# Kernel tuning notes

Hardware: AMD Instinct MI355X
Metric: run time of the kernel (lower is better)

## Reference

```python
import jax, jax.numpy as jnp
import numpy as np

V, D, NH, NL, HID = 128000, 512, 8, 2, 1408
HD = D // NH
HALF = HD // 2
B, T, NLAB, LBL = 4, 508, 5, 4
EPS = 1e-5


def setup_inputs() -> dict:
    key = jax.random.key(0)
    ks = jax.random.split(key, 16)
    g = lambda k, sh: (jax.random.normal(k, sh, jnp.float32) * 0.02)
    return {
        "input_ids": jax.random.randint(ks[0], (B, T), 0, V),
        "label_ids": jax.random.randint(ks[1], (NLAB, LBL), 0, V),
        "emb": g(ks[2], (V, D)),
        "wq": g(ks[3], (NL, D, D)),
        "wk": g(ks[4], (NL, D, D)),
        "wv": g(ks[5], (NL, D, D)),
        "wo": g(ks[6], (NL, D, D)),
        "w1": g(ks[7], (NL, D, HID)),
        "w2": g(ks[8], (NL, HID, D)),
        "w3": g(ks[9], (NL, D, HID)),
        "attn_norm_w": jnp.ones((NL, D), jnp.float32),
        "ffn_norm_w": jnp.ones((NL, D), jnp.float32),
        "final_norm_w": jnp.ones((D,), jnp.float32),
        "lm_head": g(ks[10], (D, V)),
    }


def _rmsnorm(x, w):
    return x * jax.lax.rsqrt(jnp.mean(x * x, axis=-1, keepdims=True) + EPS) * w


def _score(input_ids, label_ids, emb, wq, wk, wv, wo, w1, w2, w3,
           attn_norm_w, ffn_norm_w, final_norm_w, lm_head):
    Bc, Tc = input_ids.shape
    nl, Lc = label_ids.shape
    S = Tc + Lc
    # pad_id is None in the original (tokenizer attr missing) -> all lengths == T.
    # Causal attention => one forward over [prefix || label] equals the per-token re-forwards.
    ctx = jnp.concatenate([
        jnp.broadcast_to(input_ids[None], (nl, Bc, Tc)),
        jnp.broadcast_to(label_ids[:, None, :], (nl, Bc, Lc)),
    ], axis=-1).reshape(nl * Bc, S)
    N = nl * Bc

    h = emb[ctx]  # [N, S, D]

    # RoPE tables
    pos = jnp.arange(S, dtype=jnp.float32)
    freqs = 1.0 / (10000.0 ** (jnp.arange(HALF, dtype=jnp.float32) / HALF))
    ang = pos[:, None] * freqs[None, :]  # [S, HALF]
    cos = jnp.cos(ang)[None, :, None, :]
    sin = jnp.sin(ang)[None, :, None, :]

    def rope(x):  # x: [N, S, NH, HD]
        x1, x2 = x[..., :HALF], x[..., HALF:]
        return jnp.concatenate([x1 * cos - x2 * sin, x1 * sin + x2 * cos], axis=-1)

    causal = jnp.tril(jnp.ones((S, S), dtype=bool))
    scale = 1.0 / jnp.sqrt(jnp.float32(HD))

    for l in range(NL):
        xn = _rmsnorm(h, attn_norm_w[l])
        q = rope((xn @ wq[l]).reshape(N, S, NH, HD))
        k = rope((xn @ wk[l]).reshape(N, S, NH, HD))
        v = (xn @ wv[l]).reshape(N, S, NH, HD)
        scores = jnp.einsum('nqhd,nkhd->nhqk', q, k) * scale
        scores = jnp.where(causal, scores, jnp.float32(-1e9))
        p = jax.nn.softmax(scores, axis=-1)
        o = jnp.einsum('nhqk,nkhd->nqhd', p, v).reshape(N, S, D)
        h = h + o @ wo[l]
        xn = _rmsnorm(h, ffn_norm_w[l])
        h = h + (jax.nn.silu(xn @ w1[l]) * (xn @ w3[l])) @ w2[l]

    h = _rmsnorm(h, final_norm_w)
    # Only positions T-1 .. T+L-2 predict label tokens; project only those.
    hs = h[:, Tc - 1:Tc - 1 + Lc, :]                    # [N, L, D]
    lp = jax.nn.log_softmax(hs @ lm_head, axis=-1)      # [N, L, V]
    lp = lp.reshape(nl, Bc, Lc, V)
    idx = jnp.broadcast_to(label_ids[:, None, :, None], (nl, Bc, Lc, 1))
    tok_lp = jnp.take_along_axis(lp, idx, axis=-1)[..., 0]  # [nl, B, L]
    return tok_lp.sum(axis=-1).T.astype(jnp.float32)        # [B, num_labels]


def reference(input_ids, label_ids, emb, wq, wk, wv, wo, w1, w2, w3,
              attn_norm_w, ffn_norm_w, final_norm_w, lm_head):
    return _score(input_ids, label_ids, emb, wq, wk, wv, wo, w1, w2, w3,
                  attn_norm_w, ffn_norm_w, final_norm_w, lm_head)
```

## Files before the change

kernel.cpp:

```cpp
#include <hip/hip_runtime.h>
#include <math.h>

typedef unsigned short u16;
typedef unsigned int u32;

namespace {
constexpr int kV = 128000, kD = 512, kNH = 8, kNL = 2, kHID = 1408;
constexpr int kHD = 64, kB = 4, kT = 508, kNLAB = 5, kLBL = 4;
constexpr int kS = 512;
constexpr int kNSeq = kNLAB * kB;
constexpr int kNS = kNSeq * kS;
constexpr int kQK = 1024;
constexpr float kEps = 1e-5f;
constexpr int kNChunk = 2000;
constexpr int kPad = 56;
constexpr int kStr = 72;
constexpr int kPL = 3211264;
constexpr int oWQ = 0, oWK = 262144, oWV = 524288, oWO = 786432;
constexpr int oW1 = 1048576, oW3 = 1769472, oW2 = 2490368;
}

typedef __attribute__((ext_vector_type(8))) short bf16x8;
typedef __attribute__((ext_vector_type(4))) float f32x4;

__device__ inline u32 pk2(float lo, float hi) {
  u32 ul = __builtin_bit_cast(u32, lo);
  u32 uh = __builtin_bit_cast(u32, hi);
  ul += 0x7fffu + ((ul >> 16) & 1u);
  uh += 0x7fffu + ((uh >> 16) & 1u);
  return (ul >> 16) | (uh & 0xffff0000u);
}
__device__ inline u16 bf1(float x) {
  u32 u = __builtin_bit_cast(u32, x);
  u += 0x7fffu + ((u >> 16) & 1u);
  return (u16)(u >> 16);
}
__device__ inline float bf2f(u16 u) {
  return __builtin_bit_cast(float, ((u32)u) << 16);
}
__device__ inline void gload16(const void* g, void* l) {
  __builtin_amdgcn_global_load_lds(
      (const __attribute__((address_space(1))) void*)g,
      (__attribute__((address_space(3))) void*)l, 16, 0, 0);
}
__device__ inline size_t tix(int Kt, int row, int k) {
  return ((size_t)(row >> 7) * Kt + (k >> 6)) * 8192 +
         ((((k >> 4) & 3) * 2 + ((k >> 3) & 1)) * 128 + (row & 127)) * 8 + (k & 7);
}

__global__ __launch_bounds__(256) void k_wtrans_all(const float* __restrict__ wq,
                                                    const float* __restrict__ wk,
                                                    const float* __restrict__ wv,
                                                    const float* __restrict__ wo,
                                                    const float* __restrict__ w1,
                                                    const float* __restrict__ w3,
                                                    const float* __restrict__ w2,
                                                    u16* __restrict__ wT) {
  int bid = blockIdx.x;
  int l = bid / 3136, r = bid % 3136;
  const float* src; u16* dst; int K, N, gxw, t; float scale = 1.f;
  if (r < 1024) {
    int w = r >> 8; t = r & 255; K = 512; N = 512; gxw = 16;
    src = (w == 0 ? wq : w == 1 ? wk : w == 2 ? wv : wo) + (size_t)l * 262144;
    dst = wT + (size_t)l * kPL + w * 262144;
    if (w == 0) scale = 0.125f;
  } else if (r < 2432) {
    int rr = r - 1024; int w = rr / 704; t = rr - w * 704; K = 512; N = 1408; gxw = 44;
    src = (w ? w3 : w1) + (size_t)l * 720896;
    dst = wT + (size_t)l * kPL + (w ? oW3 : oW1);
  } else {
    t = r - 2432; K = 1408; N = 512; gxw = 16;
    src = w2 + (size_t)l * 720896;
    dst = wT + (size_t)l * kPL + oW2;
  }
  int bn = (t % gxw) * 32, bk = (t / gxw) * 32;
  __shared__ float tb[32][33];
  int tid = threadIdx.x;
  int rr2 = tid >> 3, c4 = (tid & 7) * 4;
  float4 v = *(const float4*)(src + (size_t)(bk + rr2) * N + bn + c4);
  tb[rr2][c4 + 0] = v.x * scale; tb[rr2][c4 + 1] = v.y * scale;
  tb[rr2][c4 + 2] = v.z * scale; tb[rr2][c4 + 3] = v.w * scale;
  __syncthreads();
  uint2 o;
  o.x = pk2(tb[c4 + 0][rr2], tb[c4 + 1][rr2]);
  o.y = pk2(tb[c4 + 2][rr2], tb[c4 + 3][rr2]);
  *(uint2*)&dst[tix(K >> 6, bn + rr2, bk + c4)] = o;
}

__global__ void k_embed(const int* __restrict__ input_ids, const int* __restrict__ label_ids,
                        const float* __restrict__ emb, float* __restrict__ h) {
  int row = blockIdx.x;
  int n = row / kS, s = row - n * kS;
  int lab = n / kB, b = n - lab * kB;
  int tok = (s < kT) ? input_ids[b * kT + s] : label_ids[lab * kLBL + (s - kT)];
  const float4* src = (const float4*)(emb + (size_t)tok * kD);
  float4* dst = (float4*)(h + (size_t)row * kD);
  for (int i = threadIdx.x; i < kD / 4; i += blockDim.x) dst[i] = src[i];
}

__global__ __launch_bounds__(256) void k_rmsnorm(const float* __restrict__ x,
                                                 const float* __restrict__ w,
                                                 u16* __restrict__ y) {
  int row = blockIdx.x;
  int tid = threadIdx.x;
  const float* xr = x + (size_t)row * kD;
  int i = tid * 2;
  float v0 = xr[i], v1 = xr[i + 1];
  float ss = v0 * v0 + v1 * v1;
  #pragma unroll
  for (int o = 1; o < 64; o <<= 1) ss += __shfl_xor(ss, o);
  __shared__ float wsum[4];
  int lane = tid & 63, wid = tid >> 6;
  if (lane == 0) wsum[wid] = ss;
  __syncthreads();
  float tot = wsum[0] + wsum[1] + wsum[2] + wsum[3];
  float inv = rsqrtf(tot / (float)kD + kEps);
  *(u32*)&y[tix(8, row, i)] = pk2(v0 * inv * w[i], v1 * inv * w[i + 1]);
}

__global__ __launch_bounds__(256) void k_gemm_qkv(const u16* __restrict__ A,
                                                  const u16* __restrict__ Bt,
                                                  u16* __restrict__ qk,
                                                  u16* __restrict__ vT) {
  __shared__ u16 As[8192];
  __shared__ u16 Bs[8192];
  int wg = (blockIdx.x & 7) * 120 + (blockIdx.x >> 3);
  int by = wg / 12, bx = wg - by * 12;
  int row0 = by * 128, col0 = bx * 128;
  int tid = threadIdx.x;
  int wave = tid >> 6, lane = tid & 63;
  int wm = wave >> 1, wn = wave & 1;
  int l15 = lane & 15, l16 = lane >> 4;
  f32x4 acc[4][4];
  #pragma unroll
  for (int i = 0; i < 4; i++)
    #pragma unroll
    for (int j = 0; j < 4; j++) acc[i][j] = (f32x4){0.f, 0.f, 0.f, 0.f};

  for (int kt = 0; kt < 8; kt++) {
    const u16* Ab = A  + ((size_t)(row0 >> 7) * 8 + kt) * 8192;
    const u16* Bb = Bt + ((size_t)(col0 >> 7) * 8 + kt) * 8192;
    #pragma unroll
    for (int i = 0; i < 4; i++) {
      int off = ((wave * 2 + (i >> 1)) * 128 + (i & 1) * 64) * 8;
      gload16(Ab + off + (size_t)lane * 8, (char*)As + off * 2);
      gload16(Bb + off + (size_t)lane * 8, (char*)Bs + off * 2);
    }
    __syncthreads();
    #pragma unroll
    for (int h = 0; h < 2; h++) {
      bf16x8 af[4], bfr[4];
      #pragma unroll
      for (int mf = 0; mf < 4; mf++)
        af[mf] = *(const bf16x8*)&As[((h * 4 + l16) * 128 + wm * 64 + mf * 16 + l15) * 8];
      #pragma unroll
      for (int nf = 0; nf < 4; nf++)
        bfr[nf] = *(const bf16x8*)&Bs[((h * 4 + l16) * 128 + wn * 64 + nf * 16 + l15) * 8];
      #pragma unroll
      for (int mf = 0; mf < 4; mf++)
        #pragma unroll
        for (int nf = 0; nf < 4; nf++)
          acc[mf][nf] = __builtin_amdgcn_mfma_f32_16x16x32_bf16(af[mf], bfr[nf], acc[mf][nf], 0, 0, 0);
    }
    __syncthreads();
  }

  if (bx < 8) {
    #pragma unroll
    for (int nf = 0; nf < 2; nf++) {
      int d = nf * 16 + l15;
      float fr = __expf(-0.2878231366242558f * (float)d);
      #pragma unroll
      for (int mf = 0; mf < 4; mf++)
        #pragma unroll
        for (int r = 0; r < 4; r++) {
          int row = row0 + wm * 64 + mf * 16 + l16 * 4 + r;
          int s = row & (kS - 1);
          float sn, cs;
          __sincosf((float)s * fr, &sn, &cs);
          float x1 = acc[mf][nf][r], x2 = acc[mf][nf + 2][r];
          size_t base = (size_t)row * kQK + col0 + wn * 64 + nf * 16 + l15;
          qk[base]      = bf1(x1 * cs - x2 * sn);
          qk[base + 32] = bf1(x1 * sn + x2 * cs);
        }
    }
  } else {
    int n = row0 >> 9;
    #pragma unroll
    for (int mf = 0; mf < 4; mf++) {
      int s0 = (row0 & (kS - 1)) + wm * 64 + mf * 16 + l16 * 4;
      #pragma unroll
      for (int nf = 0; nf < 4; nf++) {
        int v = (bx - 8) * 128 + wn * 64 + nf * 16 + l15;
        int hh = v >> 6, d = v & 63;
        uint2 ow;
        ow.x = pk2(acc[mf][nf][0], acc[mf][nf][1]);
        ow.y = pk2(acc[mf][nf][2], acc[mf][nf][3]);
        *(uint2*)&vT[(size_t)((n * kNH + hh) * kHD + d) * kS + s0] = ow;
      }
    }
  }
}

__global__ __launch_bounds__(256) void k_gemm_n64(const u16* __restrict__ A,
                                                  const u16* __restrict__ Bt,
                                                  float* __restrict__ C,
                                                  int Kt, int N) {
  __shared__ u16 As[8192];
  __shared__ u16 Bs[4096];
  int nwg = gridDim.x;
  int wg = (blockIdx.x & 7) * (nwg >> 3) + (blockIdx.x >> 3);
  int by = wg >> 3, bx = wg & 7;
  int row0 = by * 128, col0 = bx * 64;
  int p = col0 >> 7, half = (col0 >> 6) & 1;
  int tid = threadIdx.x;
  int wave = tid >> 6, lane = tid & 63;
  int l15 = lane & 15, l16 = lane >> 4;
  f32x4 acc[2][4];
  #pragma unroll
  for (int i = 0; i < 2; i++)
    #pragma unroll
    for (int j = 0; j < 4; j++) acc[i][j] = (f32x4){0.f, 0.f, 0.f, 0.f};

  for (int kt = 0; kt < Kt; kt++) {
    const u16* Ab = A  + ((size_t)(row0 >> 7) * Kt + kt) * 8192;
    const u16* Bb = Bt + ((size_t)p * Kt + kt) * 8192;
    #pragma unroll
    for (int i = 0; i < 4; i++) {
      int off = ((wave * 2 + (i >> 1)) * 128 + (i & 1) * 64) * 8;
      gload16(Ab + off + (size_t)lane * 8, (char*)As + off * 2);
    }
    #pragma unroll
    for (int sl = 0; sl < 2; sl++) {
      int ch = wave * 2 + sl;
      gload16(Bb + (ch * 128 + half * 64) * 8 + (size_t)lane * 8,
              (char*)Bs + (ch * 64) * 16);
    }
    __syncthreads();
    #pragma unroll
    for (int h = 0; h < 2; h++) {
      bf16x8 af[2], bfr[4];
      #pragma unroll
      for (int mf = 0; mf < 2; mf++)
        af[mf] = *(const bf16x8*)&As[((h * 4 + l16) * 128 + wave * 32 + mf * 16 + l15) * 8];
      #pragma unroll
      for (int nf = 0; nf < 4; nf++)
        bfr[nf] = *(const bf16x8*)&Bs[((h * 4 + l16) * 64 + nf * 16 + l15) * 8];
      #pragma unroll
      for (int mf = 0; mf < 2; mf++)
        #pragma unroll
        for (int nf = 0; nf < 4; nf++)
          acc[mf][nf] = __builtin_amdgcn_mfma_f32_16x16x32_bf16(af[mf], bfr[nf], acc[mf][nf], 0, 0, 0);
    }
    __syncthreads();
  }
  #pragma unroll
  for (int mf = 0; mf < 2; mf++)
    #pragma unroll
    for (int nf = 0; nf < 4; nf++)
      #pragma unroll
      for (int r = 0; r < 4; r++) {
        int row = row0 + wave * 32 + mf * 16 + l16 * 4 + r;
        int col = col0 + nf * 16 + l15;
        C[(size_t)row * N + col] += acc[mf][nf][r];
      }
}

__global__ __launch_bounds__(256) void k_ffn13_bf16(const u16* __restrict__ A,
                                                    const u16* __restrict__ W1t,
                                                    const u16* __restrict__ W3t,
                                                    u16* __restrict__ act) {
  __shared__ u16 As[8192];
  __shared__ u16 B1[8192];
  __shared__ u16 B2[8192];
  int wg = (blockIdx.x & 7) * 110 + (blockIdx.x >> 3);
  int by = wg / 11, bx = wg - by * 11;
  int row0 = by * 128, col0 = bx * 128;
  int tid = threadIdx.x;
  int wave = tid >> 6, lane = tid & 63;
  int wm = wave >> 1, wn = wave & 1;
  int l15 = lane & 15, l16 = lane >> 4;
  f32x4 acc1[4][4], acc2[4][4];
  #pragma unroll
  for (int i = 0; i < 4; i++)
    #pragma unroll
    for (int j = 0; j < 4; j++) {
      acc1[i][j] = (f32x4){0.f, 0.f, 0.f, 0.f};
      acc2[i][j] = (f32x4){0.f, 0.f, 0.f, 0.f};
    }

  for (int kt = 0; kt < 8; kt++) {
    const u16* Ab  = A   + ((size_t)(row0 >> 7) * 8 + kt) * 8192;
    const u16* B1b = W1t + ((size_t)(col0 >> 7) * 8 + kt) * 8192;
    const u16* B3b = W3t + ((size_t)(col0 >> 7) * 8 + kt) * 8192;
    #pragma unroll
    for (int i = 0; i < 4; i++) {
      int off = ((wave * 2 + (i >> 1)) * 128 + (i & 1) * 64) * 8;
      gload16(Ab  + off + (size_t)lane * 8, (char*)As + off * 2);
      gload16(B1b + off + (size_t)lane * 8, (char*)B1 + off * 2);
      gload16(B3b + off + (size_t)lane * 8, (char*)B2 + off * 2);
    }
    __syncthreads();
    #pragma unroll
    for (int h = 0; h < 2; h++) {
      bf16x8 af[4], b1f[4], b2f[4];
      #pragma unroll
      for (int mf = 0; mf < 4; mf++)
        af[mf] = *(const bf16x8*)&As[((h * 4 + l16) * 128 + wm * 64 + mf * 16 + l15) * 8];
      #pragma unroll
      for (int nf = 0; nf < 4; nf++) {
        b1f[nf] = *(const bf16x8*)&B1[((h * 4 + l16) * 128 + wn * 64 + nf * 16 + l15) * 8];
        b2f[nf] = *(const bf16x8*)&B2[((h * 4 + l16) * 128 + wn * 64 + nf * 16 + l15) * 8];
      }
      #pragma unroll
      for (int mf = 0; mf < 4; mf++)
        #pragma unroll
        for (int nf = 0; nf < 4; nf++) {
          acc1[mf][nf] = __builtin_amdgcn_mfma_f32_16x16x32_bf16(af[mf], b1f[nf], acc1[mf][nf], 0, 0, 0);
          acc2[mf][nf] = __builtin_amdgcn_mfma_f32_16x16x32_bf16(af[mf], b2f[nf], acc2[mf][nf], 0, 0, 0);
        }
    }
    __syncthreads();
  }
  #pragma unroll
  for (int mf = 0; mf < 4; mf++)
    #pragma unroll
    for (int nf = 0; nf < 4; nf++)
      #pragma unroll
      for (int r = 0; r < 4; r++) {
        int row = row0 + wm * 64 + mf * 16 + l16 * 4 + r;
        int col = col0 + wn * 64 + nf * 16 + l15;
        float aa = acc1[mf][nf][r];
        float sg = 1.f / (1.f + __expf(-aa));
        act[tix(22, row, col)] = bf1(aa * sg * acc2[mf][nf][r]);
      }
}

__global__ __launch_bounds__(256) void k_attn_mfma(const u16* __restrict__ qk,
                                                   const u16* __restrict__ vT,
                                                   u16* __restrict__ o) {
  int qt = blockIdx.x;
  int nh = blockIdx.y;
  int hh = nh & (kNH - 1), n = nh >> 3;
  int tid = threadIdx.x;
  int wq = tid >> 6, lane = tid & 63;
  int l15 = lane & 15, l16 = lane >> 4;
  __shared__ u16 Ks[64 * kStr];
  __shared__ u16 Vt[64 * kStr];
  __shared__ u16 Ps[4][16 * kStr];
  int q0 = qt * 64;
  int qrow = q0 + wq * 16 + l15;

  bf16x8 qf[2];
  {
    const u16* qg = qk + (size_t)(n * kS + qrow) * kQK + hh * kHD;
    qf[0] = *(const bf16x8*)(qg + l16 * 8);
    qf[1] = *(const bf16x8*)(qg + 32 + l16 * 8);
  }

  f32x4 oacc[4];
  #pragma unroll
  for (int i = 0; i < 4; i++) oacc[i] = (f32x4){0.f, 0.f, 0.f, 0.f};
  float m_run = -1e30f, l_run = 0.f;

  int skv = tid & 63, sd0 = (tid >> 6) * 16;
  const u16* vTh = vT + (size_t)((n * kNH + hh) * kHD) * kS;

  for (int jt = 0; jt <= qt; jt++) {
    int j0 = jt * 64;
    __syncthreads();
    {
      size_t gb = (size_t)(n * kS + j0 + skv) * kQK + 512 + hh * kHD + sd0;
      const u16* kg = qk + gb;
      *(uint4*)&Ks[skv * kStr + sd0]     = *(const uint4*)kg;
      *(uint4*)&Ks[skv * kStr + sd0 + 8] = *(const uint4*)(kg + 8);
      const u16* vg = vTh + (size_t)skv * kS + j0 + sd0;
      *(uint4*)&Vt[skv * kStr + sd0]     = *(const uint4*)vg;
      *(uint4*)&Vt[skv * kStr + sd0 + 8] = *(const uint4*)(vg + 8);
    }
    __syncthreads();

    f32x4 st[4];
    #pragma unroll
    for (int kt = 0; kt < 4; kt++) {
      bf16x8 ka0 = *(const bf16x8*)&Ks[(kt * 16 + l15) * kStr + l16 * 8];
      bf16x8 ka1 = *(const bf16x8*)&Ks[(kt * 16 + l15) * kStr + 32 + l16 * 8];
      f32x4 c = (f32x4){0.f, 0.f, 0.f, 0.f};
      c = __builtin_amdgcn_mfma_f32_16x16x32_bf16(ka0, qf[0], c, 0, 0, 0);
      c = __builtin_amdgcn_mfma_f32_16x16x32_bf16(ka1, qf[1], c, 0, 0, 0);
      st[kt] = c;
    }

    float mx = m_run;
    #pragma unroll
    for (int kt = 0; kt < 4; kt++)
      #pragma unroll
      for (int r = 0; r < 4; r++) {
        int kvg = j0 + kt * 16 + l16 * 4 + r;
        if (kvg > qrow) st[kt][r] = -1e30f;
        mx = fmaxf(mx, st[kt][r]);
      }
    mx = fmaxf(mx, __shfl_xor(mx, 16));
    mx = fmaxf(mx, __shfl_xor(mx, 32));
    float sc = __expf(m_run - mx);
    float p[4][4];
    float rs = 0.f;
    #pragma unroll
    for (int kt = 0; kt < 4; kt++)
      #pragma unroll
      for (int r = 0; r < 4; r++) { p[kt][r] = __expf(st[kt][r] - mx); rs += p[kt][r]; }
    rs += __shfl_xor(rs, 16);
    rs += __shfl_xor(rs, 32);
    l_run = l_run * sc + rs;
    m_run = mx;
    #pragma unroll
    for (int dt = 0; dt < 4; dt++)
      #pragma unroll
      for (int r = 0; r < 4; r++) oacc[dt][r] *= sc;

    #pragma unroll
    for (int kt = 0; kt < 4; kt++) {
      uint2 w2;
      w2.x = pk2(p[kt][0], p[kt][1]);
      w2.y = pk2(p[kt][2], p[kt][3]);
      *(uint2*)&Ps[wq][l15 * kStr + kt * 16 + l16 * 4] = w2;
    }
    asm volatile("s_waitcnt lgkmcnt(0)" ::: "memory");
    __builtin_amdgcn_sched_barrier(0);

    bf16x8 pf0 = *(const bf16x8*)&Ps[wq][l15 * kStr + l16 * 8];
    bf16x8 pf1 = *(const bf16x8*)&Ps[wq][l15 * kStr + 32 + l16 * 8];
    #pragma unroll
    for (int dt = 0; dt < 4; dt++) {
      bf16x8 va0 = *(const bf16x8*)&Vt[(dt * 16 + l15) * kStr + l16 * 8];
      bf16x8 va1 = *(const bf16x8*)&Vt[(dt * 16 + l15) * kStr + 32 + l16 * 8];
      oacc[dt] = __builtin_amdgcn_mfma_f32_16x16x32_bf16(va0, pf0, oacc[dt], 0, 0, 0);
      oacc[dt] = __builtin_amdgcn_mfma_f32_16x16x32_bf16(va1, pf1, oacc[dt], 0, 0, 0);
    }
  }

  float inv = 1.f / l_run;
  int rowIdx = n * kS + qrow;
  #pragma unroll
  for (int dt = 0; dt < 4; dt++) {
    uint2 ow;
    ow.x = pk2(oacc[dt][0] * inv, oacc[dt][1] * inv);
    ow.y = pk2(oacc[dt][2] * inv, oacc[dt][3] * inv);
    size_t base = ((size_t)(rowIdx >> 7) * 8 + hh) * 8192 +
                  (size_t)(((dt * 2 + ((l16 >> 1) & 1)) * 128 + (rowIdx & 127)) * 8 + (l16 & 1) * 4);
    *(uint2*)&o[base] = ow;
  }
}

__global__ __launch_bounds__(256) void k_rms_gather(const float* __restrict__ x,
                                                    const float* __restrict__ w,
                                                    u16* __restrict__ hs) {
  int r = blockIdx.x;
  int n = r >> 2, li = r & 3;
  int row = n * kS + (kT - 1 + li);
  int tid = threadIdx.x;
  const float* xr = x + (size_t)row * kD;
  int i = tid * 2;
  float v0 = xr[i], v1 = xr[i + 1];
  float ss = v0 * v0 + v1 * v1;
  #pragma unroll
  for (int o = 1; o < 64; o <<= 1) ss += __shfl_xor(ss, o);
  __shared__ float wsum[4];
  int lane = tid & 63, wid = tid >> 6;
  if (lane == 0) wsum[wid] = ss;
  __syncthreads();
  float tot = wsum[0] + wsum[1] + wsum[2] + wsum[3];
  float inv = rsqrtf(tot / (float)kD + kEps);
  *(u32*)&hs[(size_t)r * kD + i] = pk2(v0 * inv * w[i], v1 * inv * w[i + 1]);
}

__global__ __launch_bounds__(256) void k_logits_mfma(const u16* __restrict__ hs,
                                                     const float* __restrict__ lm,
                                                     float* __restrict__ part) {
  __shared__ u16 As[80 * kPad];
  __shared__ u16 Bs[4 * 256 * 8];
  int tid = threadIdx.x;
  int wave = tid >> 6, lane = tid & 63;
  int l15 = lane & 15, l16 = lane >> 4;
  int col0 = blockIdx.x * 256;
  f32x4 acc[5][4];
  #pragma unroll
  for (int i = 0; i < 5; i++)
    #pragma unroll
    for (int j = 0; j < 4; j++) acc[i][j] = (f32x4){0.f, 0.f, 0.f, 0.f};

  int arow = tid >> 1, ahalf = tid & 1;
  int bkp = tid >> 4, bf4 = tid & 15;
  int slot = bkp >> 2, ksub = (2 * bkp) & 7;

  for (int k0 = 0; k0 < kD; k0 += 32) {
    if (tid < 160) {
      const u16* ag = hs + (size_t)arow * kD + k0 + ahalf * 16;
      *(uint4*)&As[arow * kPad + ahalf * 16]     = *(const uint4*)ag;
      *(uint4*)&As[arow * kPad + ahalf * 16 + 8] = *(const uint4*)(ag + 8);
    }
    #pragma unroll
    for (int t = 0; t < 4; t++) {
      int colq = bf4 + 16 * t;
      const float* bg = lm + (size_t)(k0 + 2 * bkp) * kV + col0 + colq * 4;
      float4 lo = *(const float4*)bg;
      float4 hi = *(const float4*)(bg + kV);
      *(u32*)&Bs[(slot * 256 + colq * 4 + 0) * 8 + ksub] = pk2(lo.x, hi.x);
      *(u32*)&Bs[(slot * 256 + colq * 4 + 1) * 8 + ksub] = pk2(lo.y, hi.y);
      *(u32*)&Bs[(slot * 256 + colq * 4 + 2) * 8 + ksub] = pk2(lo.z, hi.z);
      *(u32*)&Bs[(slot * 256 + colq * 4 + 3) * 8 + ksub] = pk2(lo.w, hi.w);
    }
    __syncthreads();
    bf16x8 af[5], bfr[4];
    #pragma unroll
    for (int mf = 0; mf < 5; mf++)
      af[mf] = *(const bf16x8*)&As[(mf * 16 + l15) * kPad + l16 * 8];
    #pragma unroll
    for (int nf = 0; nf < 4; nf++)
      bfr[nf] = *(const bf16x8*)&Bs[(l16 * 256 + wave * 64 + nf * 16 + l15) * 8];
    #pragma unroll
    for (int mf = 0; mf < 5; mf++)
      #pragma unroll
      for (int nf = 0; nf < 4; nf++)
        acc[mf][nf] = __builtin_amdgcn_mfma_f32_16x16x32_bf16(af[mf], bfr[nf], acc[mf][nf], 0, 0, 0);
    __syncthreads();
  }

  int chunk = blockIdx.x * 4 + wave;
  #pragma unroll
  for (int mf = 0; mf < 5; mf++)
    #pragma unroll
    for (int r = 0; r < 4; r++) {
      float mx = fmaxf(fmaxf(acc[mf][0][r], acc[mf][1][r]),
                       fmaxf(acc[mf][2][r], acc[mf][3][r]));
      #pragma unroll
      for (int off = 1; off < 16; off <<= 1) mx = fmaxf(mx, __shfl_xor(mx, off));
      float se = expf(acc[mf][0][r] - mx) + expf(acc[mf][1][r] - mx) +
                 expf(acc[mf][2][r] - mx) + expf(acc[mf][3][r] - mx);
      #pragma unroll
      for (int off = 1; off < 16; off <<= 1) se += __shfl_xor(se, off);
      if (l15 == 0) {
        int row = mf * 16 + l16 * 4 + r;
        size_t pi = ((size_t)row * kNChunk + chunk) * 2;
        part[pi] = mx; part[pi + 1] = se;
      }
    }
}

__global__ __launch_bounds__(64) void k_final(const float* __restrict__ part,
                                              const u16* __restrict__ hs,
                                              const float* __restrict__ lm,
                                              const int* __restrict__ label_ids,
                                              float* __restrict__ out) {
  int n = blockIdx.x;
  int lab = n / kB, b = n - lab * kB;
  int lane = threadIdx.x;
  float res = 0.f;
  for (int li = 0; li < kLBL; li++) {
    int r = n * kLBL + li;
    int tok = label_ids[lab * kLBL + li];
    float dv = 0.f;
    for (int d2 = lane; d2 < kD; d2 += 64)
      dv += bf2f(hs[(size_t)r * kD + d2]) * lm[(size_t)d2 * kV + tok];
    #pragma unroll
    for (int o2 = 1; o2 < 64; o2 <<= 1) dv += __shfl_xor(dv, o2);
    const float* pr = part + (size_t)r * kNChunk * 2;
    float mx = -1e30f;
    for (int c = lane; c < kNChunk; c += 64) mx = fmaxf(mx, pr[c * 2]);
    #pragma unroll
    for (int o2 = 1; o2 < 64; o2 <<= 1) mx = fmaxf(mx, __shfl_xor(mx, o2));
    float sum = 0.f;
    for (int c = lane; c < kNChunk; c += 64) sum += pr[c * 2 + 1] * expf(pr[c * 2] - mx);
    #pragma unroll
    for (int o2 = 1; o2 < 64; o2 <<= 1) sum += __shfl_xor(sum, o2);
    res += dv - (mx + logf(sum));
  }
  if (lane == 0) out[b * kNLAB + lab] = res;
}

extern "C" void kernel_launch(void* const* d_in, const int* in_sizes, int n_in,
                              void* d_out, int out_size, void* d_ws, size_t ws_size,
                              hipStream_t stream) {
  const int*   input_ids    = (const int*)d_in[0];
  const int*   label_ids    = (const int*)d_in[1];
  const float* emb          = (const float*)d_in[2];
  const float* wq           = (const float*)d_in[3];
  const float* wk           = (const float*)d_in[4];
  const float* wv           = (const float*)d_in[5];
  const float* wo           = (const float*)d_in[6];
  const float* w1           = (const float*)d_in[7];
  const float* w2           = (const float*)d_in[8];
  const float* w3           = (const float*)d_in[9];
  const float* attn_norm_w  = (const float*)d_in[10];
  const float* ffn_norm_w   = (const float*)d_in[11];
  const float* final_norm_w = (const float*)d_in[12];
  const float* lm_head      = (const float*)d_in[13];
  float* out = (float*)d_out;

  char* ws = (char*)d_ws;
  float* h    = (float*)(ws);
  u16*   xn   = (u16*)(ws + 20971520);
  u16*   qk   = (u16*)(ws + 31457280);
  u16*   vT   = (u16*)(ws + 52428800);
  u16*   big  = (u16*)(ws + 62914560);
  u16*   hsb  = (u16*)(ws + 91750400);
  float* part = (float*)(ws + 91832320);
  u16*   wT   = (u16*)(ws + 93112640);

  k_wtrans_all<<<2 * 3136, 256, 0, stream>>>(wq, wk, wv, wo, w1, w3, w2, wT);
  k_embed<<<kNS, 128, 0, stream>>>(input_ids, label_ids, emb, h);

  for (int l = 0; l < kNL; l++) {
    u16* base = wT + (size_t)l * kPL;
    k_rmsnorm<<<kNS, 256, 0, stream>>>(h, attn_norm_w + (size_t)l * kD, xn);
    k_gemm_qkv<<<960, 256, 0, stream>>>(xn, base + oWQ, qk, vT);
    dim3 gattn(kS / 64, kNSeq * kNH);
    k_attn_mfma<<<gattn, 256, 0, stream>>>(qk, vT, big);
    k_gemm_n64<<<640, 256, 0, stream>>>(big, base + oWO, h, 8, kD);
    k_rmsnorm<<<kNS, 256, 0, stream>>>(h, ffn_norm_w + (size_t)l * kD, xn);
    k_ffn13_bf16<<<880, 256, 0, stream>>>(xn, base + oW1, base + oW3, big);
    k_gemm_n64<<<640, 256, 0, stream>>>(big, base + oW2, h, 22, kD);
  }

  k_rms_gather<<<kNSeq * kLBL, 256, 0, stream>>>(h, final_norm_w, hsb);
  k_logits_mfma<<<kV / 256, 256, 0, stream>>>(hsb, lm_head, part);
  k_final<<<kNSeq, 64, 0, stream>>>(part, hsb, lm_head, label_ids, out);
}
```

Baseline: 529.2 us.

## Fuse embedding with first RMSNorm, widen attention q-tile, narrow logits tiles

Three unrelated changes. The embedding gather now also computes the first attention RMSNorm, which removes one full pass over h. The attention kernel now gives each wave 32 query rows, so one K/V tile load in shared memory serves twice as many rows, at the cost of fewer blocks and more registers. The logits kernel uses 128-column tiles instead of 256, doubling the block count (and the partial chunk buffer) to improve occupancy, with the workspace offset moved to fit.

```diff
diff --git a/kernel.cpp b/kernel.cpp
--- a/kernel.cpp
+++ b/kernel.cpp
@@ -12,7 +12,7 @@
 constexpr int kNS = kNSeq * kS;
 constexpr int kQK = 1024;
 constexpr float kEps = 1e-5f;
-constexpr int kNChunk = 2000;
+constexpr int kNChunk = 4000;
 constexpr int kPad = 56;
 constexpr int kStr = 72;
 constexpr int kPL = 3211264;
@@ -87,15 +87,31 @@
   *(uint2*)&dst[tix(K >> 6, bn + rr2, bk + c4)] = o;
 }
 
-__global__ void k_embed(const int* __restrict__ input_ids, const int* __restrict__ label_ids,
-                        const float* __restrict__ emb, float* __restrict__ h) {
+__global__ __launch_bounds__(256) void k_embed_rms(const int* __restrict__ input_ids,
+                                                   const int* __restrict__ label_ids,
+                                                   const float* __restrict__ emb,
+                                                   const float* __restrict__ w,
+                                                   float* __restrict__ h,
+                                                   u16* __restrict__ xn) {
   int row = blockIdx.x;
   int n = row / kS, s = row - n * kS;
   int lab = n / kB, b = n - lab * kB;
   int tok = (s < kT) ? input_ids[b * kT + s] : label_ids[lab * kLBL + (s - kT)];
-  const float4* src = (const float4*)(emb + (size_t)tok * kD);
-  float4* dst = (float4*)(h + (size_t)row * kD);
-  for (int i = threadIdx.x; i < kD / 4; i += blockDim.x) dst[i] = src[i];
+  int tid = threadIdx.x;
+  const float* src = emb + (size_t)tok * kD;
+  int i = tid * 2;
+  float v0 = src[i], v1 = src[i + 1];
+  float ss = v0 * v0 + v1 * v1;
+  #pragma unroll
+  for (int o = 1; o < 64; o <<= 1) ss += __shfl_xor(ss, o);
+  __shared__ float wsum[4];
+  int lane = tid & 63, wid = tid >> 6;
+  if (lane == 0) wsum[wid] = ss;
+  __syncthreads();
+  float tot = wsum[0] + wsum[1] + wsum[2] + wsum[3];
+  float inv = rsqrtf(tot / (float)kD + kEps);
+  *(float2*)&h[(size_t)row * kD + i] = make_float2(v0, v1);
+  *(u32*)&xn[tix(8, row, i)] = pk2(v0 * inv * w[i], v1 * inv * w[i + 1]);
 }
 
 __global__ __launch_bounds__(256) void k_rmsnorm(const float* __restrict__ x,
@@ -339,7 +355,7 @@
 __global__ __launch_bounds__(256) void k_attn_mfma(const u16* __restrict__ qk,
                                                    const u16* __restrict__ vT,
                                                    u16* __restrict__ o) {
-  int qt = blockIdx.x;
+  int qb = blockIdx.x;
   int nh = blockIdx.y;
   int hh = nh & (kNH - 1), n = nh >> 3;
   int tid = threadIdx.x;
@@ -347,26 +363,29 @@
   int l15 = lane & 15, l16 = lane >> 4;
   __shared__ u16 Ks[64 * kStr];
   __shared__ u16 Vt[64 * kStr];
-  __shared__ u16 Ps[4][16 * kStr];
-  int q0 = qt * 64;
-  int qrow = q0 + wq * 16 + l15;
-
-  bf16x8 qf[2];
-  {
-    const u16* qg = qk + (size_t)(n * kS + qrow) * kQK + hh * kHD;
-    qf[0] = *(const bf16x8*)(qg + l16 * 8);
-    qf[1] = *(const bf16x8*)(qg + 32 + l16 * 8);
-  }
-
-  f32x4 oacc[4];
-  #pragma unroll
-  for (int i = 0; i < 4; i++) oacc[i] = (f32x4){0.f, 0.f, 0.f, 0.f};
-  float m_run = -1e30f, l_run = 0.f;
+  __shared__ u16 Ps[4][32 * kStr];
+  int qbase = qb * 128 + wq * 32;
+
+  bf16x8 qf[2][2];
+  #pragma unroll
+  for (int g = 0; g < 2; g++) {
+    const u16* qg = qk + (size_t)(n * kS + qbase + g * 16 + l15) * kQK + hh * kHD;
+    qf[g][0] = *(const bf16x8*)(qg + l16 * 8);
+    qf[g][1] = *(const bf16x8*)(qg + 32 + l16 * 8);
+  }
+
+  f32x4 oacc[2][4];
+  #pragma unroll
+  for (int g = 0; g < 2; g++)
+    #pragma unroll
+    for (int i = 0; i < 4; i++) oacc[g][i] = (f32x4){0.f, 0.f, 0.f, 0.f};
+  float m_run[2] = {-1e30f, -1e30f}, l_run[2] = {0.f, 0.f};
 
   int skv = tid & 63, sd0 = (tid >> 6) * 16;
   const u16* vTh = vT + (size_t)((n * kNH + hh) * kHD) * kS;
-
-  for (int jt = 0; jt <= qt; jt++) {
+  int ntile = 2 * qb + 2;
+
+  for (int jt = 0; jt < ntile; jt++) {
     int j0 = jt * 64;
     __syncthreads();
     {
@@ -380,75 +399,88 @@
     }
     __syncthreads();
 
-    f32x4 st[4];
-    #pragma unroll
-    for (int kt = 0; kt < 4; kt++) {
-      bf16x8 ka0 = *(const bf16x8*)&Ks[(kt * 16 + l15) * kStr + l16 * 8];
-      bf16x8 ka1 = *(const bf16x8*)&Ks[(kt * 16 + l15) * kStr + 32 + l16 * 8];
-      f32x4 c = (f32x4){0.f, 0.f, 0.f, 0.f};
-      c = __builtin_amdgcn_mfma_f32_16x16x32_bf16(ka0, qf[0], c, 0, 0, 0);
-      c = __builtin_amdgcn_mfma_f32_16x16x32_bf16(ka1, qf[1], c, 0, 0, 0);
-      st[kt] = c;
-    }
-
-    float mx = m_run;
-    #pragma unroll
-    for (int kt = 0; kt < 4; kt++)
-      #pragma unroll
-      for (int r = 0; r < 4; r++) {
-        int kvg = j0 + kt * 16 + l16 * 4 + r;
-        if (kvg > qrow) st[kt][r] = -1e30f;
-        mx = fmaxf(mx, st[kt][r]);
-      }
-    mx = fmaxf(mx, __shfl_xor(mx, 16));
-    mx = fmaxf(mx, __shfl_xor(mx, 32));
-    float sc = __expf(m_run - mx);
-    float p[4][4];
-    float rs = 0.f;
-    #pragma unroll
-    for (int kt = 0; kt < 4; kt++)
-      #pragma unroll
-      for (int r = 0; r < 4; r++) { p[kt][r] = __expf(st[kt][r] - mx); rs += p[kt][r]; }
-    rs += __shfl_xor(rs, 16);
-    rs += __shfl_xor(rs, 32);
-    l_run = l_run * sc + rs;
-    m_run = mx;
-    #pragma unroll
-    for (int dt = 0; dt < 4; dt++)
-      #pragma unroll
-      for (int r = 0; r < 4; r++) oacc[dt][r] *= sc;
-
-    #pragma unroll
-    for (int kt = 0; kt < 4; kt++) {
-      uint2 w2;
-      w2.x = pk2(p[kt][0], p[kt][1]);
-      w2.y = pk2(p[kt][2], p[kt][3]);
-      *(uint2*)&Ps[wq][l15 * kStr + kt * 16 + l16 * 4] = w2;
+    #pragma unroll
+    for (int g = 0; g < 2; g++) {
+      int qrow = qbase + g * 16 + l15;
+      f32x4 st[4];
+      #pragma unroll
+      for (int kt = 0; kt < 4; kt++) {
+        bf16x8 ka0 = *(const bf16x8*)&Ks[(kt * 16 + l15) * kStr + l16 * 8];
+        bf16x8 ka1 = *(const bf16x8*)&Ks[(kt * 16 + l15) * kStr + 32 + l16 * 8];
+        f32x4 c = (f32x4){0.f, 0.f, 0.f, 0.f};
+        c = __builtin_amdgcn_mfma_f32_16x16x32_bf16(ka0, qf[g][0], c, 0, 0, 0);
+        c = __builtin_amdgcn_mfma_f32_16x16x32_bf16(ka1, qf[g][1], c, 0, 0, 0);
+        st[kt] = c;
+      }
+      float mx = m_run[g];
+      #pragma unroll
+      for (int kt = 0; kt < 4; kt++)
+        #pragma unroll
+        for (int r = 0; r < 4; r++) {
+          int kvg = j0 + kt * 16 + l16 * 4 + r;
+          if (kvg > qrow) st[kt][r] = -1e30f;
+          mx = fmaxf(mx, st[kt][r]);
+        }
+      mx = fmaxf(mx, __shfl_xor(mx, 16));
+      mx = fmaxf(mx, __shfl_xor(mx, 32));
+      float sc = __expf(m_run[g] - mx);
+      float p[4][4];
+      float rs = 0.f;
+      #pragma unroll
+      for (int kt = 0; kt < 4; kt++)
+        #pragma unroll
+        for (int r = 0; r < 4; r++) { p[kt][r] = __expf(st[kt][r] - mx); rs += p[kt][r]; }
+      rs += __shfl_xor(rs, 16);
+      rs += __shfl_xor(rs, 32);
+      l_run[g] = l_run[g] * sc + rs;
+      m_run[g] = mx;
+      #pragma unroll
+      for (int dt = 0; dt < 4; dt++)
+        #pragma unroll
+        for (int r = 0; r < 4; r++) oacc[g][dt][r] *= sc;
+
+      #pragma unroll
+      for (int kt = 0; kt < 4; kt++) {
+        uint2 w2;
+        w2.x = pk2(p[kt][0], p[kt][1]);
+        w2.y = pk2(p[kt][2], p[kt][3]);
+        *(uint2*)&Ps[wq][(g * 16 + l15) * kStr + kt * 16 + l16 * 4] = w2;
+      }
     }
     asm volatile("s_waitcnt lgkmcnt(0)" ::: "memory");
     __builtin_amdgcn_sched_barrier(0);
 
-    bf16x8 pf0 = *(const bf16x8*)&Ps[wq][l15 * kStr + l16 * 8];
-    bf16x8 pf1 = *(const bf16x8*)&Ps[wq][l15 * kStr + 32 + l16 * 8];
+    bf16x8 pf[2][2];
+    #pragma unroll
+    for (int g = 0; g < 2; g++) {
+      pf[g][0] = *(const bf16x8*)&Ps[wq][(g * 16 + l15) * kStr + l16 * 8];
+      pf[g][1] = *(const bf16x8*)&Ps[wq][(g * 16 + l15) * kStr + 32 + l16 * 8];
+    }
     #pragma unroll
     for (int dt = 0; dt < 4; dt++) {
       bf16x8 va0 = *(const bf16x8*)&Vt[(dt * 16 + l15) * kStr + l16 * 8];
       bf16x8 va1 = *(const bf16x8*)&Vt[(dt * 16 + l15) * kStr + 32 + l16 * 8];
-      oacc[dt] = __builtin_amdgcn_mfma_f32_16x16x32_bf16(va0, pf0, oacc[dt], 0, 0, 0);
-      oacc[dt] = __builtin_amdgcn_mfma_f32_16x16x32_bf16(va1, pf1, oacc[dt], 0, 0, 0);
-    }
-  }
-
-  float inv = 1.f / l_run;
-  int rowIdx = n * kS + qrow;
-  #pragma unroll
-  for (int dt = 0; dt < 4; dt++) {
-    uint2 ow;
-    ow.x = pk2(oacc[dt][0] * inv, oacc[dt][1] * inv);
-    ow.y = pk2(oacc[dt][2] * inv, oacc[dt][3] * inv);
-    size_t base = ((size_t)(rowIdx >> 7) * 8 + hh) * 8192 +
-                  (size_t)(((dt * 2 + ((l16 >> 1) & 1)) * 128 + (rowIdx & 127)) * 8 + (l16 & 1) * 4);
-    *(uint2*)&o[base] = ow;
+      #pragma unroll
+      for (int g = 0; g < 2; g++) {
+        oacc[g][dt] = __builtin_amdgcn_mfma_f32_16x16x32_bf16(va0, pf[g][0], oacc[g][dt], 0, 0, 0);
+        oacc[g][dt] = __builtin_amdgcn_mfma_f32_16x16x32_bf16(va1, pf[g][1], oacc[g][dt], 0, 0, 0);
+      }
+    }
+  }
+
+  #pragma unroll
+  for (int g = 0; g < 2; g++) {
+    float inv = 1.f / l_run[g];
+    int rowIdx = n * kS + qbase + g * 16 + l15;
+    #pragma unroll
+    for (int dt = 0; dt < 4; dt++) {
+      uint2 ow;
+      ow.x = pk2(oacc[g][dt][0] * inv, oacc[g][dt][1] * inv);
+      ow.y = pk2(oacc[g][dt][2] * inv, oacc[g][dt][3] * inv);
+      size_t base = ((size_t)(rowIdx >> 7) * 8 + hh) * 8192 +
+                    (size_t)(((dt * 2 + ((l16 >> 1) & 1)) * 128 + (rowIdx & 127)) * 8 + (l16 & 1) * 4);
+      *(uint2*)&o[base] = ow;
+    }
   }
 }
 
@@ -478,16 +510,16 @@
                                                      const float* __restrict__ lm,
                                                      float* __restrict__ part) {
   __shared__ u16 As[80 * kPad];
-  __shared__ u16 Bs[4 * 256 * 8];
+  __shared__ u16 Bs[4 * 128 * 8];
   int tid = threadIdx.x;
   int wave = tid >> 6, lane = tid & 63;
   int l15 = lane & 15, l16 = lane >> 4;
-  int col0 = blockIdx.x * 256;
-  f32x4 acc[5][4];
+  int col0 = blockIdx.x * 128;
+  f32x4 acc[5][2];
   #pragma unroll
   for (int i = 0; i < 5; i++)
     #pragma unroll
-    for (int j = 0; j < 4; j++) acc[i][j] = (f32x4){0.f, 0.f, 0.f, 0.f};
+    for (int j = 0; j < 2; j++) acc[i][j] = (f32x4){0.f, 0.f, 0.f, 0.f};
 
   int arow = tid >> 1, ahalf = tid & 1;
   int bkp = tid >> 4, bf4 = tid & 15;
@@ -500,28 +532,28 @@
       *(uint4*)&As[arow * kPad + ahalf * 16 + 8] = *(const uint4*)(ag + 8);
     }
     #pragma unroll
-    for (int t = 0; t < 4; t++) {
+    for (int t = 0; t < 2; t++) {
       int colq = bf4 + 16 * t;
       const float* bg = lm + (size_t)(k0 + 2 * bkp) * kV + col0 + colq * 4;
       float4 lo = *(const float4*)bg;
       float4 hi = *(const float4*)(bg + kV);
-      *(u32*)&Bs[(slot * 256 + colq * 4 + 0) * 8 + ksub] = pk2(lo.x, hi.x);
-      *(u32*)&Bs[(slot * 256 + colq * 4 + 1) * 8 + ksub] = pk2(lo.y, hi.y);
-      *(u32*)&Bs[(slot * 256 + colq * 4 + 2) * 8 + ksub] = pk2(lo.z, hi.z);
-      *(u32*)&Bs[(slot * 256 + colq * 4 + 3) * 8 + ksub] = pk2(lo.w, hi.w);
-    }
-    __syncthreads();
-    bf16x8 af[5], bfr[4];
+      *(u32*)&Bs[(slot * 128 + colq * 4 + 0) * 8 + ksub] = pk2(lo.x, hi.x);
+      *(u32*)&Bs[(slot * 128 + colq * 4 + 1) * 8 + ksub] = pk2(lo.y, hi.y);
+      *(u32*)&Bs[(slot * 128 + colq * 4 + 2) * 8 + ksub] = pk2(lo.z, hi.z);
+      *(u32*)&Bs[(slot * 128 + colq * 4 + 3) * 8 + ksub] = pk2(lo.w, hi.w);
+    }
+    __syncthreads();
+    bf16x8 af[5], bfr[2];
     #pragma unroll
     for (int mf = 0; mf < 5; mf++)
       af[mf] = *(const bf16x8*)&As[(mf * 16 + l15) * kPad + l16 * 8];
     #pragma unroll
-    for (int nf = 0; nf < 4; nf++)
-      bfr[nf] = *(const bf16x8*)&Bs[(l16 * 256 + wave * 64 + nf * 16 + l15) * 8];
+    for (int nf = 0; nf < 2; nf++)
+      bfr[nf] = *(const bf16x8*)&Bs[(l16 * 128 + wave * 32 + nf * 16 + l15) * 8];
     #pragma unroll
     for (int mf = 0; mf < 5; mf++)
       #pragma unroll
-      for (int nf = 0; nf < 4; nf++)
+      for (int nf = 0; nf < 2; nf++)
         acc[mf][nf] = __builtin_amdgcn_mfma_f32_16x16x32_bf16(af[mf], bfr[nf], acc[mf][nf], 0, 0, 0);
     __syncthreads();
   }
@@ -531,12 +563,10 @@
   for (int mf = 0; mf < 5; mf++)
     #pragma unroll
     for (int r = 0; r < 4; r++) {
-      float mx = fmaxf(fmaxf(acc[mf][0][r], acc[mf][1][r]),
-                       fmaxf(acc[mf][2][r], acc[mf][3][r]));
+      float mx = fmaxf(acc[mf][0][r], acc[mf][1][r]);
       #pragma unroll
       for (int off = 1; off < 16; off <<= 1) mx = fmaxf(mx, __shfl_xor(mx, off));
-      float se = expf(acc[mf][0][r] - mx) + expf(acc[mf][1][r] - mx) +
-                 expf(acc[mf][2][r] - mx) + expf(acc[mf][3][r] - mx);
+      float se = expf(acc[mf][0][r] - mx) + expf(acc[mf][1][r] - mx);
       #pragma unroll
       for (int off = 1; off < 16; off <<= 1) se += __shfl_xor(se, off);
       if (l15 == 0) {
@@ -605,16 +635,17 @@
   u16*   big  = (u16*)(ws + 62914560);
   u16*   hsb  = (u16*)(ws + 91750400);
   float* part = (float*)(ws + 91832320);
-  u16*   wT   = (u16*)(ws + 93112640);
+  u16*   wT   = (u16*)(ws + 94392320);
 
   k_wtrans_all<<<2 * 3136, 256, 0, stream>>>(wq, wk, wv, wo, w1, w3, w2, wT);
-  k_embed<<<kNS, 128, 0, stream>>>(input_ids, label_ids, emb, h);
+  k_embed_rms<<<kNS, 256, 0, stream>>>(input_ids, label_ids, emb, attn_norm_w, h, xn);
 
   for (int l = 0; l < kNL; l++) {
     u16* base = wT + (size_t)l * kPL;
-    k_rmsnorm<<<kNS, 256, 0, stream>>>(h, attn_norm_w + (size_t)l * kD, xn);
+    if (l > 0)
+      k_rmsnorm<<<kNS, 256, 0, stream>>>(h, attn_norm_w + (size_t)l * kD, xn);
     k_gemm_qkv<<<960, 256, 0, stream>>>(xn, base + oWQ, qk, vT);
-    dim3 gattn(kS / 64, kNSeq * kNH);
+    dim3 gattn(kS / 128, kNSeq * kNH);
     k_attn_mfma<<<gattn, 256, 0, stream>>>(qk, vT, big);
     k_gemm_n64<<<640, 256, 0, stream>>>(big, base + oWO, h, 8, kD);
     k_rmsnorm<<<kNS, 256, 0, stream>>>(h, ffn_norm_w + (size_t)l * kD, xn);
@@ -623,6 +654,6 @@
   }
 
   k_rms_gather<<<kNSeq * kLBL, 256, 0, stream>>>(h, final_norm_w, hsb);
-  k_logits_mfma<<<kV / 256, 256, 0, stream>>>(hsb, lm_head, part);
+  k_logits_mfma<<<kV / 128, 256, 0, stream>>>(hsb, lm_head, part);
   k_final<<<kNSeq, 64, 0, stream>>>(part, hsb, lm_head, label_ids, out);
 }
```

New measurement: 571.0 us. +7.9%, slower.
